# Performance work log

Measured on AMD Instinct MI355X. Metric: run time of the kernel, lower is better.

## Reference

```python
import jax, jax.numpy as jnp
import numpy as np

B = 8192          # batch size
D = 1024          # embedding dim
N_CLASSES = 7     # 7 emotion labels


def setup_inputs() -> dict:
    key = jax.random.key(0)
    k1, k2, k3, k4 = jax.random.split(key, 4)
    return {
        "label": jax.random.randint(k1, (B,), 0, N_CLASSES),
        "s_t": jax.random.normal(k2, (B, D), dtype=jnp.float32),
        "s_v": jax.random.normal(k3, (B, D), dtype=jnp.float32),
        "s_a": jax.random.normal(k4, (B, D), dtype=jnp.float32),
    }


def _single_modal_loss(label, anchor, a_cls, a_m, m_1, m_2):
    # anchor embedding and its norm
    anc = a_m[anchor]                                  # [D]
    anc_norm = jnp.linalg.norm(anc)
    # batched cosine similarity of anchor vs every row of m_1 and m_2
    def cos(m):
        return (m @ anc) / (jnp.linalg.norm(m, axis=1) * anc_norm)  # [B]
    c = cos(m_1) + cos(m_2)                            # [B]
    not_anchor = jnp.arange(label.shape[0]) != anchor
    same = label == label[anchor]
    pos_mask = not_anchor & same
    neg_mask = not_anchor & ~same
    # original code normalizes by full class count (anchor included)
    pos_num = jnp.sum(label == a_cls).astype(c.dtype)
    neg_num = label.shape[0] - pos_num
    pos_score = jnp.sum(jnp.where(pos_mask, c, 0.0)) / pos_num
    neg_score = jnp.sum(jnp.where(neg_mask, c, 0.0)) / neg_num
    return 2.0 - pos_score + neg_score


def reference(label, s_t, s_v, s_a):
    # first class (starting from 0) with more than one sample, like the while loop
    counts = jax.ops.segment_sum(jnp.ones_like(label), label, num_segments=N_CLASSES)
    a_cls = jnp.argmax(counts > 1)
    # deterministic anchor: first index of that class
    anchor = jnp.argmax(label == a_cls)
    t1 = _single_modal_loss(label, anchor, a_cls, s_t, s_v, s_a)
    t2 = _single_modal_loss(label, anchor, a_cls, s_a, s_t, s_v)
    t3 = _single_modal_loss(label, anchor, a_cls, s_v, s_a, s_t)
    return (t1 + t2 + t3) / 3.0
```

## Files before the change

### kernel.cpp

```cpp
#include <hip/hip_runtime.h>

#define NCLS 7

struct Hdr {
    int   anchor;
    int   a_cls;
    float pos_num;
    float neg_num;
    float inv_at;
    float inv_av;
    float inv_aa;
    int   pad;
};

__device__ __forceinline__ float dot4(float4 a, float4 b) {
    return a.x * b.x + a.y * b.y + a.z * b.z + a.w * b.w;
}

__global__ __launch_bounds__(1024) void prep_kernel(
    const int* __restrict__ label,
    const float* __restrict__ s_t,
    const float* __restrict__ s_v,
    const float* __restrict__ s_a,
    int B, int D, float* __restrict__ ws)
{
    const int tid  = threadIdx.x;
    const int w    = tid >> 6;
    const int lane = tid & 63;

    int cnt[NCLS];
    int mn[NCLS];
#pragma unroll
    for (int k = 0; k < NCLS; ++k) { cnt[k] = 0; mn[k] = 0x7fffffff; }

    const int4* lab4 = (const int4*)label;
    const int n4 = B >> 2;
    for (int j = tid; j < n4; j += 1024) {
        int4 L = lab4[j];
        const int base = j << 2;
        int ls[4] = { L.x, L.y, L.z, L.w };
#pragma unroll
        for (int e = 0; e < 4; ++e) {
#pragma unroll
            for (int k = 0; k < NCLS; ++k) {
                if (ls[e] == k) { cnt[k]++; mn[k] = min(mn[k], base + e); }
            }
        }
    }
    for (int i = (n4 << 2) + tid; i < B; i += 1024) {
        int l = label[i];
#pragma unroll
        for (int k = 0; k < NCLS; ++k)
            if (l == k) { cnt[k]++; mn[k] = min(mn[k], i); }
    }

#pragma unroll
    for (int k = 0; k < NCLS; ++k) {
        for (int off = 32; off; off >>= 1) {
            cnt[k] += __shfl_xor(cnt[k], off);
            mn[k]   = min(mn[k], __shfl_xor(mn[k], off));
        }
    }

    __shared__ int   s_cnt[16][NCLS], s_mn[16][NCLS];
    __shared__ int   s_anchor;
    __shared__ float s_norm[12];
    if (lane == 0) {
#pragma unroll
        for (int k = 0; k < NCLS; ++k) { s_cnt[w][k] = cnt[k]; s_mn[w][k] = mn[k]; }
    }
    __syncthreads();

    if (tid == 0) {
        int hist[NCLS], mini[NCLS];
#pragma unroll
        for (int k = 0; k < NCLS; ++k) {
            int hc = 0, mc = 0x7fffffff;
            for (int q = 0; q < 16; ++q) { hc += s_cnt[q][k]; mc = min(mc, s_mn[q][k]); }
            hist[k] = hc; mini[k] = mc;
        }
        int c = 0;
#pragma unroll
        for (int k = NCLS - 1; k >= 0; --k) if (hist[k] > 1) c = k;
        s_anchor = mini[c];

        Hdr* h = (Hdr*)ws;
        h->anchor  = mini[c];
        h->a_cls   = c;
        float pn   = (float)hist[c];
        h->pos_num = pn;
        h->neg_num = (float)B - pn;
    }
    __syncthreads();

    const int anchor = s_anchor;
    if (w < 12) {
        const int rw = w >> 2, qw = w & 3;
        const float* src = (rw == 0) ? s_t : (rw == 1) ? s_v : s_a;
        const float4* row = (const float4*)(src + (size_t)anchor * D);
        const int nvec = D >> 2;
        float s = 0.f;
        for (int j = qw * 64 + lane; j < nvec; j += 256) {
            float4 x = row[j];
            s += dot4(x, x);
        }
        for (int off = 32; off; off >>= 1) s += __shfl_xor(s, off);
        if (lane == 0) s_norm[w] = s;
    }
    __syncthreads();
    if (tid < 3)
        ((float*)ws)[4 + tid] = rsqrtf(s_norm[4 * tid] + s_norm[4 * tid + 1] +
                                       s_norm[4 * tid + 2] + s_norm[4 * tid + 3]);
}

__global__ __launch_bounds__(256) void main_kernel(
    const int* __restrict__ label,
    const float* __restrict__ s_t,
    const float* __restrict__ s_v,
    const float* __restrict__ s_a,
    int B, int D, float* __restrict__ ws)
{
    const Hdr* h = (const Hdr*)ws;
    float2* partials = (float2*)(ws + 16);

    const int r    = blockIdx.x;
    const int tid  = threadIdx.x;
    const int w    = tid >> 6;
    const int lane = tid & 63;

    const int lab    = label[r];
    const int anchor = h->anchor;

    const float4* rt = (const float4*)(s_t + (size_t)r * D);
    const float4* rv = (const float4*)(s_v + (size_t)r * D);
    const float4* ra = (const float4*)(s_a + (size_t)r * D);
    const float4* at = (const float4*)(s_t + (size_t)anchor * D);
    const float4* av = (const float4*)(s_v + (size_t)anchor * D);
    const float4* aa = (const float4*)(s_a + (size_t)anchor * D);

    float dt_a = 0.f, dt_v = 0.f, sq_t = 0.f;
    float dv_t = 0.f, dv_a = 0.f, sq_v = 0.f;
    float da_t = 0.f, da_v = 0.f, sq_a = 0.f;

    const int nvec = D >> 2;
    for (int j = tid; j < nvec; j += 256) {
        float4 t  = rt[j], v  = rv[j], a  = ra[j];
        float4 bt = at[j], bv = av[j], ba = aa[j];
        dt_a += dot4(t, ba);
        dt_v += dot4(t, bv);
        sq_t += dot4(t, t);
        dv_t += dot4(v, bt);
        dv_a += dot4(v, ba);
        sq_v += dot4(v, v);
        da_t += dot4(a, bt);
        da_v += dot4(a, bv);
        sq_a += dot4(a, a);
    }

    for (int off = 32; off; off >>= 1) {
        sq_t += __shfl_xor(sq_t, off);
        sq_v += __shfl_xor(sq_v, off);
        sq_a += __shfl_xor(sq_a, off);
    }
    __shared__ float red_sq[4][3];
    __shared__ float red_c[4];
    if (lane == 0) {
        red_sq[w][0] = sq_t; red_sq[w][1] = sq_v; red_sq[w][2] = sq_a;
    }
    __syncthreads();

    const float SQ_t = red_sq[0][0] + red_sq[1][0] + red_sq[2][0] + red_sq[3][0];
    const float SQ_v = red_sq[0][1] + red_sq[1][1] + red_sq[2][1] + red_sq[3][1];
    const float SQ_a = red_sq[0][2] + red_sq[1][2] + red_sq[2][2] + red_sq[3][2];
    const float inv_t = rsqrtf(SQ_t);
    const float inv_v = rsqrtf(SQ_v);
    const float inv_a = rsqrtf(SQ_a);

    float combined = inv_t * (dt_a * h->inv_aa + dt_v * h->inv_av)
                   + inv_v * (dv_t * h->inv_at + dv_a * h->inv_aa)
                   + inv_a * (da_t * h->inv_at + da_v * h->inv_av);

    for (int off = 32; off; off >>= 1)
        combined += __shfl_xor(combined, off);
    if (lane == 0) red_c[w] = combined;
    __syncthreads();

    if (tid == 0) {
        float rowtot = red_c[0] + red_c[1] + red_c[2] + red_c[3];
        bool isPos = (lab == h->a_cls) && (r != anchor);
        bool isNeg = (lab != h->a_cls);
        partials[r] = make_float2(isPos ? rowtot : 0.f, isNeg ? rowtot : 0.f);
    }
}

__global__ __launch_bounds__(1024) void finish_kernel(
    const float* __restrict__ ws, int B, float* __restrict__ out)
{
    const Hdr* h = (const Hdr*)ws;
    const float2* partials = (const float2*)(ws + 16);

    float p = 0.f, n = 0.f;
    for (int i = threadIdx.x; i < B; i += 1024) {
        float2 pr = partials[i];
        p += pr.x;
        n += pr.y;
    }
    for (int off = 32; off; off >>= 1) {
        p += __shfl_xor(p, off);
        n += __shfl_xor(n, off);
    }
    __shared__ float pp[16], nn[16];
    const int w = threadIdx.x >> 6, lane = threadIdx.x & 63;
    if (lane == 0) { pp[w] = p; nn[w] = n; }
    __syncthreads();
    if (threadIdx.x == 0) {
        float P = 0.f, N = 0.f;
#pragma unroll
        for (int k = 0; k < 16; ++k) { P += pp[k]; N += nn[k]; }
        out[0] = (6.0f - P / h->pos_num + N / h->neg_num) / 3.0f;
    }
}

extern "C" void kernel_launch(void* const* d_in, const int* in_sizes, int n_in,
                              void* d_out, int out_size, void* d_ws, size_t ws_size,
                              hipStream_t stream) {
    const int*   label = (const int*)d_in[0];
    const float* s_t   = (const float*)d_in[1];
    const float* s_v   = (const float*)d_in[2];
    const float* s_a   = (const float*)d_in[3];

    const int B = in_sizes[0];
    const int D = in_sizes[1] / B;

    float* ws  = (float*)d_ws;
    float* out = (float*)d_out;

    prep_kernel<<<1, 1024, 0, stream>>>(label, s_t, s_v, s_a, B, D, ws);
    main_kernel<<<B, 256, 0, stream>>>(label, s_t, s_v, s_a, B, D, ws);
    finish_kernel<<<1, 1024, 0, stream>>>(ws, B, out);
}
```

Baseline: 34.19 us.

## Map one wavefront per row and use DPP wave reductions

The main kernel now gives each 64-lane wavefront its own row, four rows per block, instead of spreading one row across a 256-thread block. This removes the shared-memory reductions and __syncthreads. Cross-lane sums now use DPP row operations plus readlane instead of shfl_xor. When D is 1024, all loads are unrolled into registers up front to raise memory-level parallelism, at the cost of higher register use per thread.

```diff
diff --git a/kernel.cpp b/kernel.cpp
--- a/kernel.cpp
+++ b/kernel.cpp
@@ -17,6 +17,17 @@
     return a.x * b.x + a.y * b.y + a.z * b.z + a.w * b.w;
 }
 
+__device__ __forceinline__ float wave_sum_dpp(float x) {
+    float t;
+    t = __int_as_float(__builtin_amdgcn_update_dpp(0, __float_as_int(x), 0x111, 0xf, 0xf, true));  x += t;
+    t = __int_as_float(__builtin_amdgcn_update_dpp(0, __float_as_int(x), 0x112, 0xf, 0xf, true));  x += t;
+    t = __int_as_float(__builtin_amdgcn_update_dpp(0, __float_as_int(x), 0x114, 0xf, 0xf, true));  x += t;
+    t = __int_as_float(__builtin_amdgcn_update_dpp(0, __float_as_int(x), 0x118, 0xf, 0xf, true));  x += t;
+    t = __int_as_float(__builtin_amdgcn_update_dpp(0, __float_as_int(x), 0x142, 0xa, 0xf, false)); x += t;
+    t = __int_as_float(__builtin_amdgcn_update_dpp(0, __float_as_int(x), 0x143, 0xc, 0xf, false)); x += t;
+    return __int_as_float(__builtin_amdgcn_readlane(__float_as_int(x), 63));
+}
+
 __global__ __launch_bounds__(1024) void prep_kernel(
     const int* __restrict__ label,
     const float* __restrict__ s_t,
@@ -123,13 +134,12 @@
     const Hdr* h = (const Hdr*)ws;
     float2* partials = (float2*)(ws + 16);
 
-    const int r    = blockIdx.x;
-    const int tid  = threadIdx.x;
-    const int w    = tid >> 6;
-    const int lane = tid & 63;
-
+    const int lane = threadIdx.x & 63;
+    const int r    = blockIdx.x * 4 + (threadIdx.x >> 6);
+    if (r >= B) return;
+
+    const int anchor = h->anchor;
     const int lab    = label[r];
-    const int anchor = h->anchor;
 
     const float4* rt = (const float4*)(s_t + (size_t)r * D);
     const float4* rv = (const float4*)(s_v + (size_t)r * D);
@@ -143,50 +153,40 @@
     float da_t = 0.f, da_v = 0.f, sq_a = 0.f;
 
     const int nvec = D >> 2;
-    for (int j = tid; j < nvec; j += 256) {
-        float4 t  = rt[j], v  = rv[j], a  = ra[j];
-        float4 bt = at[j], bv = av[j], ba = aa[j];
-        dt_a += dot4(t, ba);
-        dt_v += dot4(t, bv);
-        sq_t += dot4(t, t);
-        dv_t += dot4(v, bt);
-        dv_a += dot4(v, ba);
-        sq_v += dot4(v, v);
-        da_t += dot4(a, bt);
-        da_v += dot4(a, bv);
-        sq_a += dot4(a, a);
-    }
-
-    for (int off = 32; off; off >>= 1) {
-        sq_t += __shfl_xor(sq_t, off);
-        sq_v += __shfl_xor(sq_v, off);
-        sq_a += __shfl_xor(sq_a, off);
-    }
-    __shared__ float red_sq[4][3];
-    __shared__ float red_c[4];
+    if (nvec == 256) {
+        float4 T[4], V[4], A[4], BT[4], BV[4], BA[4];
+#pragma unroll
+        for (int it = 0; it < 4; ++it) {
+            const int j = lane + (it << 6);
+            T[it]  = rt[j];  V[it]  = rv[j];  A[it]  = ra[j];
+            BT[it] = at[j];  BV[it] = av[j];  BA[it] = aa[j];
+        }
+#pragma unroll
+        for (int it = 0; it < 4; ++it) {
+            dt_a += dot4(T[it], BA[it]);  dt_v += dot4(T[it], BV[it]);  sq_t += dot4(T[it], T[it]);
+            dv_t += dot4(V[it], BT[it]);  dv_a += dot4(V[it], BA[it]);  sq_v += dot4(V[it], V[it]);
+            da_t += dot4(A[it], BT[it]);  da_v += dot4(A[it], BV[it]);  sq_a += dot4(A[it], A[it]);
+        }
+    } else {
+        for (int j = lane; j < nvec; j += 64) {
+            float4 t  = rt[j], v  = rv[j], a  = ra[j];
+            float4 bt = at[j], bv = av[j], ba = aa[j];
+            dt_a += dot4(t, ba);  dt_v += dot4(t, bv);  sq_t += dot4(t, t);
+            dv_t += dot4(v, bt);  dv_a += dot4(v, ba);  sq_v += dot4(v, v);
+            da_t += dot4(a, bt);  da_v += dot4(a, bv);  sq_a += dot4(a, a);
+        }
+    }
+
+    const float inv_t = rsqrtf(wave_sum_dpp(sq_t));
+    const float inv_v = rsqrtf(wave_sum_dpp(sq_v));
+    const float inv_a = rsqrtf(wave_sum_dpp(sq_a));
+
+    float c = inv_t * (dt_a * h->inv_aa + dt_v * h->inv_av)
+            + inv_v * (dv_t * h->inv_at + dv_a * h->inv_aa)
+            + inv_a * (da_t * h->inv_at + da_v * h->inv_av);
+    const float rowtot = wave_sum_dpp(c);
+
     if (lane == 0) {
-        red_sq[w][0] = sq_t; red_sq[w][1] = sq_v; red_sq[w][2] = sq_a;
-    }
-    __syncthreads();
-
-    const float SQ_t = red_sq[0][0] + red_sq[1][0] + red_sq[2][0] + red_sq[3][0];
-    const float SQ_v = red_sq[0][1] + red_sq[1][1] + red_sq[2][1] + red_sq[3][1];
-    const float SQ_a = red_sq[0][2] + red_sq[1][2] + red_sq[2][2] + red_sq[3][2];
-    const float inv_t = rsqrtf(SQ_t);
-    const float inv_v = rsqrtf(SQ_v);
-    const float inv_a = rsqrtf(SQ_a);
-
-    float combined = inv_t * (dt_a * h->inv_aa + dt_v * h->inv_av)
-                   + inv_v * (dv_t * h->inv_at + dv_a * h->inv_aa)
-                   + inv_a * (da_t * h->inv_at + da_v * h->inv_av);
-
-    for (int off = 32; off; off >>= 1)
-        combined += __shfl_xor(combined, off);
-    if (lane == 0) red_c[w] = combined;
-    __syncthreads();
-
-    if (tid == 0) {
-        float rowtot = red_c[0] + red_c[1] + red_c[2] + red_c[3];
         bool isPos = (lab == h->a_cls) && (r != anchor);
         bool isNeg = (lab != h->a_cls);
         partials[r] = make_float2(isPos ? rowtot : 0.f, isNeg ? rowtot : 0.f);
@@ -235,7 +235,9 @@
     float* ws  = (float*)d_ws;
     float* out = (float*)d_out;
 
+    const int nblocks = (B + 3) / 4;
+
     prep_kernel<<<1, 1024, 0, stream>>>(label, s_t, s_v, s_a, B, D, ws);
-    main_kernel<<<B, 256, 0, stream>>>(label, s_t, s_v, s_a, B, D, ws);
+    main_kernel<<<nblocks, 256, 0, stream>>>(label, s_t, s_v, s_a, B, D, ws);
     finish_kernel<<<1, 1024, 0, stream>>>(ws, B, out);
 }
```

New measurement: 33.30 us. -2.6%, faster.
